# Kernel tuning notes

Hardware: AMD Instinct MI355X
Metric: run time of the kernel (lower is better)

The kernel has to match this reference:

```python
import jax, jax.numpy as jnp
import numpy as np
import math

B, S, D, H = 2, 2048, 1024, 16
HD = D // H  # head_dim = 64
ROPE_BASE = 100000
EPS = 1e-09


def _linear_init(key, in_f, out_f):
    std = min(1.0, math.sqrt(out_f / in_f)) / math.sqrt(in_f)
    return jax.random.normal(key, (in_f, out_f)) * std


def setup_inputs() -> dict:
    key = jax.random.key(0)
    ks = jax.random.split(key, 7)
    Q = jax.random.normal(ks[0], (B, S, D), dtype=jnp.float32)
    K = jax.random.normal(ks[1], (B, S, D), dtype=jnp.float32)
    V = jax.random.normal(ks[2], (B, S, D), dtype=jnp.float32)
    mask = jnp.tril(jnp.ones((S, S), dtype=bool))  # causal
    Wq = _linear_init(ks[3], D, D)
    Wk = _linear_init(ks[4], D, D)
    Wv = _linear_init(ks[5], D, D)
    Wo = _linear_init(ks[6], D, D)
    return {"Q": Q, "K": K, "V": V, "mask": mask,
            "Wq": Wq, "Wk": Wk, "Wv": Wv, "Wo": Wo}


def _rope_tables(seq_len, d):
    positions = jnp.arange(0, seq_len)
    freqs = ROPE_BASE ** (jnp.arange(0, d, 2) / d)
    gamma = positions[:, None] * (1.0 / freqs)[None, :]  # [t, d/2]
    return jnp.cos(gamma).astype(jnp.bfloat16), jnp.sin(gamma).astype(jnp.bfloat16)


def _apply_rope(x, cos, sin):
    # x: [..., t, d]; cos/sin: [t, d/2]
    d = x.shape[-1]
    x1, x2 = x[..., : d // 2], x[..., d // 2:]
    y1 = x1 * cos + x2 * sin
    y2 = -x1 * sin + x2 * cos
    return jnp.concatenate([y1, y2], axis=-1)


def _rms_norm(x):
    rms = jnp.sqrt(jnp.mean(jnp.square(x), axis=-1, keepdims=True) + EPS)
    return x / rms


def reference(Q, K, V, mask, Wq, Wk, Wv, Wo):
    cos, sin = _rope_tables(S, HD)
    q = jnp.dot(Q, Wq)
    k = jnp.dot(K, Wk)
    v = jnp.dot(V, Wv)
    # [B, S, D] -> [B, H, S, HD]
    split = lambda t: t.reshape(*t.shape[:-1], H, HD).swapaxes(-3, -2)
    q, k, v = split(q), split(k), split(v)
    q = _rms_norm(_apply_rope(q, cos, sin))
    k = _rms_norm(_apply_rope(k, cos, sin))
    logits = jnp.einsum('bhqd,bhkd->bhqk', q, k) / jnp.sqrt(jnp.float32(HD))
    logits = jnp.where(mask[None, None, :, :], logits, -1000000000.0)
    attn = jax.nn.softmax(logits, axis=-1)
    vals = jnp.einsum('bhqk,bhkd->bhqd', attn, v)
    # [B, H, S, HD] -> [B, S, D]
    vals = vals.swapaxes(-3, -2).reshape(B, S, D)
    return jnp.dot(vals, Wo)
```

## Files before the change

kernel.cpp:

```cpp
#include <hip/hip_runtime.h>
#include <hip/hip_bf16.h>
#include <stdint.h>

typedef __hip_bfloat16 bf16;
typedef __attribute__((ext_vector_type(8))) short short8;
typedef __attribute__((ext_vector_type(4))) short short4v;
typedef __attribute__((ext_vector_type(4))) float float4v;

static constexpr int nB = 2, nS = 2048, nD = 1024, nH = 16, nHD = 64;
static constexpr int nBS = nB * nS;

#define AS_GLOBAL __attribute__((address_space(1)))
#define AS_LDS    __attribute__((address_space(3)))

union Frag16B { short8 v; uint4 u4; uint2 u2[2]; };

__device__ __forceinline__ void gload_lds16(const void* g, void* l) {
  __builtin_amdgcn_global_load_lds((AS_GLOBAL uint32_t*)(g), (AS_LDS uint32_t*)(l), 16, 0, 0);
}

__device__ __forceinline__ float fast_exp2(float x) {
#if __has_builtin(__builtin_amdgcn_exp2f)
  return __builtin_amdgcn_exp2f(x);
#else
  float r; asm volatile("v_exp_f32 %0, %1" : "=v"(r) : "v"(x)); return r;
#endif
}

__device__ __forceinline__ void lds_barrier() {
  asm volatile("s_waitcnt lgkmcnt(0)\ns_barrier" ::: "memory");
}

__device__ __forceinline__ void lgkm_wait() {
  asm volatile("s_waitcnt lgkmcnt(0)" ::: "memory");
}

__global__ __launch_bounds__(256) void prep_kernel(
    const float* __restrict__ Qin, const float* __restrict__ Kin, const float* __restrict__ Vin,
    const float* __restrict__ Wq, const float* __restrict__ Wk,
    const float* __restrict__ Wv, const float* __restrict__ Wo,
    bf16* __restrict__ Qbf, bf16* __restrict__ Kbf, bf16* __restrict__ Vbf,
    bf16* __restrict__ WqT, bf16* __restrict__ WkT, bf16* __restrict__ WvT, bf16* __restrict__ WoT,
    bf16* __restrict__ cos_t, bf16* __restrict__ sin_t) {
  __shared__ float tile[64][65];
  int bx = blockIdx.x, t = threadIdx.x;
  if (bx < 3072) {
    int tz = bx >> 10, blk = bx & 1023;
    const float* src = tz == 0 ? Qin : tz == 1 ? Kin : Vin;
    bf16* dst = tz == 0 ? Qbf : tz == 1 ? Kbf : Vbf;
#pragma unroll
    for (int i = 0; i < 4; ++i) {
      int idx = blk * 1024 + i * 256 + t;
      float4 v = ((const float4*)src)[idx];
      union { bf16 b[4]; uint2 u; } tmp;
      tmp.b[0] = __float2bfloat16(v.x);
      tmp.b[1] = __float2bfloat16(v.y);
      tmp.b[2] = __float2bfloat16(v.z);
      tmp.b[3] = __float2bfloat16(v.w);
      ((uint2*)dst)[idx] = tmp.u;
    }
  } else if (bx < 4096) {
    int idx = bx - 3072;
    int z = idx >> 8;
    const float* W = z == 0 ? Wq : z == 1 ? Wk : z == 2 ? Wv : Wo;
    bf16* T = z == 0 ? WqT : z == 1 ? WkT : z == 2 ? WvT : WoT;
    int tk = (idx & 15) * 64, tn = ((idx >> 4) & 15) * 64;
    int c = t & 63, r0 = t >> 6;
#pragma unroll
    for (int i = 0; i < 16; ++i) {
      int r = i * 4 + r0;
      tile[r][c] = W[(size_t)(tk + r) * nD + tn + c];
    }
    __syncthreads();
#pragma unroll
    for (int i = 0; i < 16; ++i) {
      int r = i * 4 + r0;
      T[(size_t)(tn + r) * nD + tk + c] = __float2bfloat16(tile[c][r]);
    }
  } else {
    int base = (bx - 4096) * 1024 + t * 4;
#pragma unroll
    for (int i = 0; i < 4; ++i) {
      int e = base + i;
      int s = e >> 5, j = e & 31;
      float inv_freq = powf(100000.0f, -(float)(2 * j) / 64.0f);
      float g = (float)s * inv_freq;
      cos_t[e] = __float2bfloat16(cosf(g));
      sin_t[e] = __float2bfloat16(sinf(g));
    }
  }
}

__global__ __launch_bounds__(256) void gemm_qkv_kernel(
    const bf16* __restrict__ A0, const bf16* __restrict__ A1, const bf16* __restrict__ A2,
    const bf16* __restrict__ Bt0, const bf16* __restrict__ Bt1, const bf16* __restrict__ Bt2,
    bf16* __restrict__ q_h, bf16* __restrict__ k_h, bf16* __restrict__ vt_h,
    const bf16* __restrict__ cos_t, const bf16* __restrict__ sin_t) {
  const int z = blockIdx.z;
  const bf16* A  = z == 0 ? A0 : (z == 1 ? A1 : A2);
  const bf16* Bt = z == 0 ? Bt0 : (z == 1 ? Bt1 : Bt2);

  __shared__ bf16 As[128 * 64];
  __shared__ bf16 Bs[128 * 64];

  const int t = threadIdx.x;
  const int lane = t & 63;
  const int wid = t >> 6;
  const int quad = lane >> 4;
  const int l16 = lane & 15;
  const int wm = wid >> 1;
  const int wn = wid & 1;
  const int m0 = blockIdx.x * 128;
  const int n0 = blockIdx.y * 128;
  const int K = nD;
  const int rloc = lane >> 3, cl = lane & 7;
  const int cg = cl ^ rloc;

  float4v acc[4][4] = {};

  for (int kt = 0; kt < K; kt += 64) {
    __syncthreads();
#pragma unroll
    for (int p = 0; p < 4; ++p) {
      int rowbase = (p * 4 + wid) * 8;
      gload_lds16(A + (size_t)(m0 + rowbase + rloc) * K + kt + cg * 8, As + (size_t)rowbase * 64);
      gload_lds16(Bt + (size_t)(n0 + rowbase + rloc) * K + kt + cg * 8, Bs + (size_t)rowbase * 64);
    }
    __syncthreads();

#pragma unroll
    for (int ks = 0; ks < 2; ++ks) {
      Frag16B a[4], b[4];
#pragma unroll
      for (int mi = 0; mi < 4; ++mi) {
        int row = wm * 64 + mi * 16 + l16;
        int ch = (ks * 4 + quad) ^ (row & 7);
        a[mi].u4 = *(const uint4*)&As[row * 64 + ch * 8];
      }
#pragma unroll
      for (int ni = 0; ni < 4; ++ni) {
        int row = wn * 64 + ni * 16 + l16;
        int ch = (ks * 4 + quad) ^ (row & 7);
        b[ni].u4 = *(const uint4*)&Bs[row * 64 + ch * 8];
      }
#pragma unroll
      for (int mi = 0; mi < 4; ++mi)
#pragma unroll
        for (int ni = 0; ni < 4; ++ni)
          acc[mi][ni] = __builtin_amdgcn_mfma_f32_16x16x32_bf16(a[mi].v, b[ni].v, acc[mi][ni], 0, 0, 0);
    }
  }

  const int col0 = n0 + wn * 64;
  if (z <= 1) {
    bf16* dst = z ? k_h : q_h;
#pragma unroll
    for (int mi = 0; mi < 4; ++mi)
#pragma unroll
      for (int r = 0; r < 4; ++r) {
        int row = m0 + wm * 64 + mi * 16 + quad * 4 + r;
        int s = row & (nS - 1);
        float x0 = acc[mi][0][r], x1 = acc[mi][1][r], x2 = acc[mi][2][r], x3 = acc[mi][3][r];
        float y[4];
#pragma unroll
        for (int p = 0; p < 2; ++p) {
          int d = p * 16 + l16;
          float c = __bfloat162float(cos_t[s * 32 + d]);
          float sn = __bfloat162float(sin_t[s * 32 + d]);
          float xa = p ? x1 : x0, xb = p ? x3 : x2;
          y[p] = xa * c + xb * sn;
          y[p + 2] = xb * c - xa * sn;
        }
        float ss = y[0] * y[0] + y[1] * y[1] + y[2] * y[2] + y[3] * y[3];
#pragma unroll
        for (int m = 1; m <= 8; m <<= 1) ss += __shfl_xor(ss, m, 64);
        float inv = 1.0f / sqrtf(ss * (1.0f / 64.0f) + 1e-9f);
#pragma unroll
        for (int ni = 0; ni < 4; ++ni)
          dst[(size_t)row * nD + col0 + ni * 16 + l16] = __float2bfloat16(y[ni] * inv);
      }
  } else {
#pragma unroll
    for (int mi = 0; mi < 4; ++mi)
#pragma unroll
      for (int r = 0; r < 4; ++r) {
        int row = m0 + wm * 64 + mi * 16 + quad * 4 + r;
        int b = row >> 11, s = row & (nS - 1);
#pragma unroll
        for (int ni = 0; ni < 4; ++ni) {
          int col = col0 + ni * 16 + l16;
          int h = col >> 6, d = col & 63;
          vt_h[((size_t)((b * nH + h) * 64 + d)) * nS + s] = __float2bfloat16(acc[mi][ni][r]);
        }
      }
  }
}

__global__ __launch_bounds__(256) void gemm_out_kernel(
    const bf16* __restrict__ A, const bf16* __restrict__ Bt, float* __restrict__ C) {
  __shared__ bf16 As[64 * 64];
  __shared__ bf16 Bs[128 * 64];
  const int t = threadIdx.x;
  const int lane = t & 63;
  const int wid = t >> 6;
  const int quad = lane >> 4;
  const int l16 = lane & 15;
  const int wm = wid >> 1;
  const int wn = wid & 1;
  const int m0 = blockIdx.x * 64;
  const int n0 = blockIdx.y * 128;
  const int K = nD;
  const int rloc = lane >> 3, cl = lane & 7;
  const int cg = cl ^ rloc;

  float4v acc[2][4] = {};
  for (int kt = 0; kt < K; kt += 64) {
    __syncthreads();
#pragma unroll
    for (int p = 0; p < 2; ++p) {
      int rowbase = (p * 4 + wid) * 8;
      gload_lds16(A + (size_t)(m0 + rowbase + rloc) * K + kt + cg * 8, As + (size_t)rowbase * 64);
    }
#pragma unroll
    for (int p = 0; p < 4; ++p) {
      int rowbase = (p * 4 + wid) * 8;
      gload_lds16(Bt + (size_t)(n0 + rowbase + rloc) * K + kt + cg * 8, Bs + (size_t)rowbase * 64);
    }
    __syncthreads();

#pragma unroll
    for (int ks = 0; ks < 2; ++ks) {
      Frag16B a[2], b[4];
#pragma unroll
      for (int mi = 0; mi < 2; ++mi) {
        int row = wm * 32 + mi * 16 + l16;
        int ch = (ks * 4 + quad) ^ (row & 7);
        a[mi].u4 = *(const uint4*)&As[row * 64 + ch * 8];
      }
#pragma unroll
      for (int ni = 0; ni < 4; ++ni) {
        int row = wn * 64 + ni * 16 + l16;
        int ch = (ks * 4 + quad) ^ (row & 7);
        b[ni].u4 = *(const uint4*)&Bs[row * 64 + ch * 8];
      }
#pragma unroll
      for (int mi = 0; mi < 2; ++mi)
#pragma unroll
        for (int ni = 0; ni < 4; ++ni)
          acc[mi][ni] = __builtin_amdgcn_mfma_f32_16x16x32_bf16(a[mi].v, b[ni].v, acc[mi][ni], 0, 0, 0);
    }
  }
#pragma unroll
  for (int mi = 0; mi < 2; ++mi)
#pragma unroll
    for (int ni = 0; ni < 4; ++ni)
#pragma unroll
      for (int r = 0; r < 4; ++r) {
        int row = m0 + wm * 32 + mi * 16 + quad * 4 + r;
        int col = n0 + wn * 64 + ni * 16 + l16;
        C[(size_t)row * nD + col] = acc[mi][ni][r];
      }
}

static constexpr float SC = 0.18033688011112042f;

__global__ __launch_bounds__(256, 2) void attn_kernel(const bf16* __restrict__ q_h,
                                                      const bf16* __restrict__ k_h,
                                                      const bf16* __restrict__ vt_h,
                                                      bf16* __restrict__ vals) {
  __shared__ bf16 lds_buf[4 * 4096];

  const int t = threadIdx.x;
  const int lane = t & 63, wid = t >> 6, quad = lane >> 4, l16 = lane & 15;
  const int id = blockIdx.x;
  const int xcd = id & 7;
  const int j = id >> 3;
  const int jj = j & 31;
  const int bh = xcd * 4 + (jj & 3);
  const int u = jj >> 2;
  const int qt = (j < 32) ? (15 - u) : u;
  const int b = bh >> 4, h = bh & 15;

  const bf16* Kbase = k_h + ((size_t)b * nS) * nD + h * 64;
  const bf16* Vbase = vt_h + (size_t)bh * 64 * nS;

  const int row0 = t >> 3;
  const int cl = t & 7;
  const int cg = cl ^ (row0 & 7);
  const int r7 = l16 & 7;

  bf16* const scratch = lds_buf + wid * 1152;

  const int nkt = 2 * qt + 2;
  const int q0w = qt * 128 + wid * 32;

  Frag16B qf[2][2];
#pragma unroll
  for (int qs = 0; qs < 2; ++qs) {
    const bf16* qp = q_h + ((size_t)(b * nS + q0w + qs * 16 + l16)) * nD + h * 64;
    qf[qs][0].u4 = *(const uint4*)(qp + quad * 8);
    qf[qs][1].u4 = *(const uint4*)(qp + 32 + quad * 8);
  }

  uint4 kreg[2], vreg[2];
#pragma unroll
  for (int i = 0; i < 2; ++i) {
    kreg[i] = *(const uint4*)(Kbase + (size_t)(row0 + i * 32) * nD + cg * 8);
    vreg[i] = *(const uint4*)(Vbase + (size_t)(row0 + i * 32) * nS + cg * 8);
  }

  float4v o_acc[2][4] = {};
  float l_acc[2] = {0.f, 0.f};

  for (int kt = 0; kt < nkt; ++kt) {
    bf16* Kb = lds_buf + (kt & 1) * 4096;
    bf16* Vb = lds_buf + 8192 + (kt & 1) * 4096;
#pragma unroll
    for (int i = 0; i < 2; ++i) {
      *(uint4*)&Kb[(row0 + i * 32) * 64 + cl * 8] = kreg[i];
      *(uint4*)&Vb[(row0 + i * 32) * 64 + cl * 8] = vreg[i];
    }
    if (kt + 1 < nkt) {
#pragma unroll
      for (int i = 0; i < 2; ++i) {
        kreg[i] = *(const uint4*)(Kbase + (size_t)((kt + 1) * 64 + row0 + i * 32) * nD + cg * 8);
        vreg[i] = *(const uint4*)(Vbase + (size_t)(row0 + i * 32) * nS + (kt + 1) * 64 + cg * 8);
      }
    }
    lds_barrier();

    if (kt * 64 <= q0w + 31) {
      float4v st[2][4];
#pragma unroll
      for (int kt4 = 0; kt4 < 4; ++kt4) {
        int row = kt4 * 16 + l16;
        Frag16B k0, k1;
        k0.u4 = *(const uint4*)&Kb[row * 64 + ((quad ^ r7) * 8)];
        k1.u4 = *(const uint4*)&Kb[row * 64 + (((quad + 4) ^ r7) * 8)];
#pragma unroll
        for (int qs = 0; qs < 2; ++qs) {
          float4v zz = {};
          zz = __builtin_amdgcn_mfma_f32_16x16x32_bf16(k0.v, qf[qs][0].v, zz, 0, 0, 0);
          st[qs][kt4] = __builtin_amdgcn_mfma_f32_16x16x32_bf16(k1.v, qf[qs][1].v, zz, 0, 0, 0);
        }
      }

      short4v pf[2][4];
      const bool need_mask = (kt * 64 + 63) > q0w;
      if (need_mask) {
#pragma unroll
        for (int qs = 0; qs < 2; ++qs) {
          int qg = q0w + qs * 16 + l16;
#pragma unroll
          for (int kt4 = 0; kt4 < 4; ++kt4) {
            int key0 = kt * 64 + kt4 * 16 + quad * 4;
#pragma unroll
            for (int r = 0; r < 4; ++r) {
              float x = st[qs][kt4][r] * SC;
              if (key0 + r > qg) x = -12000.0f;
              float p = fast_exp2(x);
              l_acc[qs] += p;
              union { bf16 hh; short ss; } cv;
              cv.hh = __float2bfloat16(p);
              pf[qs][kt4][r] = cv.ss;
            }
          }
        }
      } else {
#pragma unroll
        for (int qs = 0; qs < 2; ++qs)
#pragma unroll
          for (int kt4 = 0; kt4 < 4; ++kt4)
#pragma unroll
            for (int r = 0; r < 4; ++r) {
              float p = fast_exp2(st[qs][kt4][r] * SC);
              l_acc[qs] += p;
              union { bf16 hh; short ss; } cv;
              cv.hh = __float2bfloat16(p);
              pf[qs][kt4][r] = cv.ss;
            }
      }

#pragma unroll
      for (int dt = 0; dt < 4; ++dt) {
        int row = dt * 16 + l16;
#pragma unroll
        for (int kt4 = 0; kt4 < 4; ++kt4) {
          int chunk = kt4 * 2 + (quad >> 1);
          union { uint2 u; short4v s; } vv;
          vv.u = *(const uint2*)&Vb[row * 64 + ((chunk ^ r7) * 8) + (quad & 1) * 4];
          o_acc[0][dt] = __builtin_amdgcn_mfma_f32_16x16x16bf16_1k(vv.s, pf[0][kt4], o_acc[0][dt], 0, 0, 0);
          o_acc[1][dt] = __builtin_amdgcn_mfma_f32_16x16x16bf16_1k(vv.s, pf[1][kt4], o_acc[1][dt], 0, 0, 0);
        }
      }
    }
  }

  lds_barrier();
#pragma unroll
  for (int qs = 0; qs < 2; ++qs) {
    float la = l_acc[qs];
    la += __shfl_xor(la, 16, 64);
    la += __shfl_xor(la, 32, 64);
    float inv_l = 1.0f / la;
#pragma unroll
    for (int dt = 0; dt < 4; ++dt) {
      union { bf16 b2[2]; uint u; } p01, p23;
      p01.b2[0] = __float2bfloat16(o_acc[qs][dt][0] * inv_l);
      p01.b2[1] = __float2bfloat16(o_acc[qs][dt][1] * inv_l);
      p23.b2[0] = __float2bfloat16(o_acc[qs][dt][2] * inv_l);
      p23.b2[1] = __float2bfloat16(o_acc[qs][dt][3] * inv_l);
      *(uint*)&scratch[l16 * 72 + dt * 16 + quad * 4] = p01.u;
      *(uint*)&scratch[l16 * 72 + dt * 16 + quad * 4 + 2] = p23.u;
    }
    lgkm_wait();
    uint4 r0 = *(const uint4*)&scratch[l16 * 72 + quad * 16];
    uint4 r1 = *(const uint4*)&scratch[l16 * 72 + quad * 16 + 8];
    int qrow = q0w + qs * 16 + l16;
    bf16* vp = vals + ((size_t)(b * nS + qrow)) * nD + h * 64 + quad * 16;
    *(uint4*)(vp) = r0;
    *(uint4*)(vp + 8) = r1;
    lgkm_wait();
  }
}

extern "C" void kernel_launch(void* const* d_in, const int* in_sizes, int n_in,
                              void* d_out, int out_size, void* d_ws, size_t ws_size,
                              hipStream_t stream) {
  const float* Qin = (const float*)d_in[0];
  const float* Kin = (const float*)d_in[1];
  const float* Vin = (const float*)d_in[2];
  const float* Wq = (const float*)d_in[4];
  const float* Wk = (const float*)d_in[5];
  const float* Wv = (const float*)d_in[6];
  const float* Wo = (const float*)d_in[7];
  float* out = (float*)d_out;

  char* ws = (char*)d_ws;
  const size_t MB = 1u << 20;
  bf16* Qbf = (bf16*)(ws + 0 * MB);
  bf16* Kbf = (bf16*)(ws + 8 * MB);
  bf16* Vbf = (bf16*)(ws + 16 * MB);
  bf16* WqT = (bf16*)(ws + 24 * MB);
  bf16* WkT = (bf16*)(ws + 26 * MB);
  bf16* WvT = (bf16*)(ws + 28 * MB);
  bf16* WoT = (bf16*)(ws + 30 * MB);
  bf16* cos_t = (bf16*)(ws + 32 * MB);
  bf16* sin_t = (bf16*)(ws + 33 * MB);
  bf16* q_h = (bf16*)(ws + 34 * MB);
  bf16* k_h = (bf16*)(ws + 42 * MB);
  bf16* vt_h = (bf16*)(ws + 50 * MB);
  bf16* vals = (bf16*)(ws + 58 * MB);

  prep_kernel<<<4160, 256, 0, stream>>>(Qin, Kin, Vin, Wq, Wk, Wv, Wo,
                                        Qbf, Kbf, Vbf, WqT, WkT, WvT, WoT, cos_t, sin_t);

  gemm_qkv_kernel<<<dim3(32, 8, 3), 256, 0, stream>>>(Qbf, Kbf, Vbf, WqT, WkT, WvT,
                                                      q_h, k_h, vt_h, cos_t, sin_t);

  attn_kernel<<<512, 256, 0, stream>>>(q_h, k_h, vt_h, vals);

  gemm_out_kernel<<<dim3(64, 8), 256, 0, stream>>>(vals, WoT, out);
}
```

Baseline: 241.2 us.

## Rewrite QKV GEMM as 256x256 tile with double-buffered LDS pipeline

The fused QKV projection GEMM moves from 128x128 tiles with 4 waves to 256x256 tiles with 8 waves. It adds a double-buffered LDS pipeline over K-steps of 32, using a packed swizzled layout, interleaved global-to-LDS prefetches, explicit waitcnt/barrier scheduling and s_setprio around MFMA bursts. The goal is to hide load latency and raise data reuse per tile. The cost is far fewer blocks (192 on a 256-CU GPU) and larger accumulator register use, which can leave CUs idle and lower occupancy.

```diff
diff --git a/kernel.cpp b/kernel.cpp
--- a/kernel.cpp
+++ b/kernel.cpp
@@ -91,74 +91,114 @@
   }
 }
 
-__global__ __launch_bounds__(256) void gemm_qkv_kernel(
+__global__ __launch_bounds__(512, 2) void gemm_qkv_kernel(
     const bf16* __restrict__ A0, const bf16* __restrict__ A1, const bf16* __restrict__ A2,
     const bf16* __restrict__ Bt0, const bf16* __restrict__ Bt1, const bf16* __restrict__ Bt2,
     bf16* __restrict__ q_h, bf16* __restrict__ k_h, bf16* __restrict__ vt_h,
     const bf16* __restrict__ cos_t, const bf16* __restrict__ sin_t) {
   const int z = blockIdx.z;
-  const bf16* A  = z == 0 ? A0 : (z == 1 ? A1 : A2);
-  const bf16* Bt = z == 0 ? Bt0 : (z == 1 ? Bt1 : Bt2);
-
-  __shared__ bf16 As[128 * 64];
-  __shared__ bf16 Bs[128 * 64];
+  const bf16* __restrict__ A  = z == 0 ? A0 : (z == 1 ? A1 : A2);
+  const bf16* __restrict__ Bt = z == 0 ? Bt0 : (z == 1 ? Bt1 : Bt2);
+
+  __shared__ bf16 As[2 * 256 * 32];
+  __shared__ bf16 Bs[2 * 256 * 32];
 
   const int t = threadIdx.x;
   const int lane = t & 63;
   const int wid = t >> 6;
   const int quad = lane >> 4;
   const int l16 = lane & 15;
-  const int wm = wid >> 1;
-  const int wn = wid & 1;
-  const int m0 = blockIdx.x * 128;
-  const int n0 = blockIdx.y * 128;
-  const int K = nD;
-  const int rloc = lane >> 3, cl = lane & 7;
-  const int cg = cl ^ rloc;
-
-  float4v acc[4][4] = {};
-
-  for (int kt = 0; kt < K; kt += 64) {
-    __syncthreads();
-#pragma unroll
-    for (int p = 0; p < 4; ++p) {
-      int rowbase = (p * 4 + wid) * 8;
-      gload_lds16(A + (size_t)(m0 + rowbase + rloc) * K + kt + cg * 8, As + (size_t)rowbase * 64);
-      gload_lds16(Bt + (size_t)(n0 + rowbase + rloc) * K + kt + cg * 8, Bs + (size_t)rowbase * 64);
-    }
-    __syncthreads();
-
-#pragma unroll
-    for (int ks = 0; ks < 2; ++ks) {
-      Frag16B a[4], b[4];
-#pragma unroll
-      for (int mi = 0; mi < 4; ++mi) {
-        int row = wm * 64 + mi * 16 + l16;
-        int ch = (ks * 4 + quad) ^ (row & 7);
-        a[mi].u4 = *(const uint4*)&As[row * 64 + ch * 8];
-      }
-#pragma unroll
-      for (int ni = 0; ni < 4; ++ni) {
-        int row = wn * 64 + ni * 16 + l16;
-        int ch = (ks * 4 + quad) ^ (row & 7);
-        b[ni].u4 = *(const uint4*)&Bs[row * 64 + ch * 8];
-      }
-#pragma unroll
-      for (int mi = 0; mi < 4; ++mi)
-#pragma unroll
-        for (int ni = 0; ni < 4; ++ni)
-          acc[mi][ni] = __builtin_amdgcn_mfma_f32_16x16x32_bf16(a[mi].v, b[ni].v, acc[mi][ni], 0, 0, 0);
-    }
-  }
+  const int wm = wid >> 2;
+  const int wn = wid & 3;
+  const int m0 = blockIdx.x * 256;
+  const int n0 = blockIdx.y * 256;
+
+  const int sc    = (t & 7) ^ ((t >> 3) & 7);
+  const int sml   = 2 * (t >> 3) + (sc >> 2);
+  const int skoff = (sc & 3) * 8;
+  const int swave = wid * 512;
+
+  const int R0a = wm * 64 + (l16 >> 1);
+  const int R0b = wn * 32 + (l16 >> 1);
+  const int cpar = (l16 & 1) * 4;
+  const int abase = R0a * 64 + (((cpar + quad) ^ (R0a & 7)) * 8);
+  const int bbase = R0b * 64 + (((cpar + quad) ^ (R0b & 7)) * 8);
+
+#define STAGE_A(KT, BUF) do { \
+    const bf16* ag_ = A + (size_t)(m0 + sml) * nD + (KT) * 32 + skoff; \
+    gload_lds16(ag_, As + (BUF) + swave); \
+    gload_lds16(ag_ + (size_t)128 * nD, As + (BUF) + 4096 + swave); \
+  } while (0)
+#define STAGE_B(KT, BUF) do { \
+    const bf16* bg_ = Bt + (size_t)(n0 + sml) * nD + (KT) * 32 + skoff; \
+    gload_lds16(bg_, Bs + (BUF) + swave); \
+    gload_lds16(bg_ + (size_t)128 * nD, Bs + (BUF) + 4096 + swave); \
+  } while (0)
+
+  float4v acc[8][4] = {};
+
+  STAGE_A(0, 0);
+  STAGE_B(0, 0);
+  STAGE_A(1, 8192);
+  asm volatile("s_waitcnt vmcnt(2)" ::: "memory");
+  __builtin_amdgcn_s_barrier();
+
+#pragma unroll 2
+  for (int T = 0; T < 32; ++T) {
+    const int cu = (T & 1) * 8192;
+    const int nx = cu ^ 8192;
+
+    if (T < 31) STAGE_B(T + 1, nx);
+    Frag16B fa[4], fb[4];
+#pragma unroll
+    for (int mi = 0; mi < 4; ++mi) fa[mi].u4 = *(const uint4*)&As[cu + abase + mi * 512];
+#pragma unroll
+    for (int ni = 0; ni < 4; ++ni) fb[ni].u4 = *(const uint4*)&Bs[cu + bbase + ni * 512];
+    __builtin_amdgcn_s_setprio(1);
+#pragma unroll
+    for (int mi = 0; mi < 4; ++mi)
+#pragma unroll
+      for (int ni = 0; ni < 4; ++ni)
+        acc[mi][ni] = __builtin_amdgcn_mfma_f32_16x16x32_bf16(fa[mi].v, fb[ni].v, acc[mi][ni], 0, 0, 0);
+    __builtin_amdgcn_s_setprio(0);
+    __builtin_amdgcn_s_barrier();
+
+    Frag16B fa2[4];
+#pragma unroll
+    for (int mi = 0; mi < 4; ++mi) fa2[mi].u4 = *(const uint4*)&As[cu + abase + (mi + 4) * 512];
+    asm volatile("s_waitcnt lgkmcnt(0)" ::: "memory");
+    __builtin_amdgcn_s_setprio(1);
+#pragma unroll
+    for (int mi = 0; mi < 2; ++mi)
+#pragma unroll
+      for (int ni = 0; ni < 4; ++ni)
+        acc[4 + mi][ni] = __builtin_amdgcn_mfma_f32_16x16x32_bf16(fa2[mi].v, fb[ni].v, acc[4 + mi][ni], 0, 0, 0);
+    __builtin_amdgcn_s_setprio(0);
+    __builtin_amdgcn_s_barrier();
+
+    if (T < 30) STAGE_A(T + 2, cu);
+    __builtin_amdgcn_s_setprio(1);
+#pragma unroll
+    for (int mi = 2; mi < 4; ++mi)
+#pragma unroll
+      for (int ni = 0; ni < 4; ++ni)
+        acc[4 + mi][ni] = __builtin_amdgcn_mfma_f32_16x16x32_bf16(fa2[mi].v, fb[ni].v, acc[4 + mi][ni], 0, 0, 0);
+    __builtin_amdgcn_s_setprio(0);
+    if (T < 30) { asm volatile("s_waitcnt vmcnt(2)" ::: "memory"); }
+    else        { asm volatile("s_waitcnt vmcnt(0)" ::: "memory"); }
+    __builtin_amdgcn_s_barrier();
+  }
+#undef STAGE_A
+#undef STAGE_B
 
   const int col0 = n0 + wn * 64;
   if (z <= 1) {
     bf16* dst = z ? k_h : q_h;
 #pragma unroll
-    for (int mi = 0; mi < 4; ++mi)
+    for (int mi = 0; mi < 8; ++mi)
 #pragma unroll
       for (int r = 0; r < 4; ++r) {
-        int row = m0 + wm * 64 + mi * 16 + quad * 4 + r;
+        int row = m0 + wm * 128 + mi * 16 + quad * 4 + r;
         int s = row & (nS - 1);
         float x0 = acc[mi][0][r], x1 = acc[mi][1][r], x2 = acc[mi][2][r], x3 = acc[mi][3][r];
         float y[4];
@@ -181,10 +221,10 @@
       }
   } else {
 #pragma unroll
-    for (int mi = 0; mi < 4; ++mi)
+    for (int mi = 0; mi < 8; ++mi)
 #pragma unroll
       for (int r = 0; r < 4; ++r) {
-        int row = m0 + wm * 64 + mi * 16 + quad * 4 + r;
+        int row = m0 + wm * 128 + mi * 16 + quad * 4 + r;
         int b = row >> 11, s = row & (nS - 1);
 #pragma unroll
         for (int ni = 0; ni < 4; ++ni) {
@@ -455,7 +495,7 @@
   prep_kernel<<<4160, 256, 0, stream>>>(Qin, Kin, Vin, Wq, Wk, Wv, Wo,
                                         Qbf, Kbf, Vbf, WqT, WkT, WvT, WoT, cos_t, sin_t);
 
-  gemm_qkv_kernel<<<dim3(32, 8, 3), 256, 0, stream>>>(Qbf, Kbf, Vbf, WqT, WkT, WvT,
+  gemm_qkv_kernel<<<dim3(16, 4, 3), 512, 0, stream>>>(Qbf, Kbf, Vbf, WqT, WkT, WvT,
                                                       q_h, k_h, vt_h, cos_t, sin_t);
 
   attn_kernel<<<512, 256, 0, stream>>>(q_h, k_h, vt_h, vals);
```

New measurement: 239.8 us. Within noise of the previous version (-0.6%).
